# Kernel optimization log

Measured on AMD Instinct MI355X. Metric: run time of the kernel, lower is better.

The kernel has to match this reference:

```python
import jax, jax.numpy as jnp
import numpy as np

N_QUBITS = 4
N_LAYERS = 2
PROJ_DIM = 64
B = 262144
C64 = jnp.complex64


def setup_inputs() -> dict:
    key = jax.random.key(0)
    ks = jax.random.split(key, 4)
    x = jax.random.normal(ks[0], (B, N_QUBITS), dtype=jnp.float32)
    # TorchLayer default init: uniform(0, 2*pi)
    weights = jax.random.uniform(ks[1], (N_LAYERS, N_QUBITS, 3), dtype=jnp.float32) * (2.0 * np.pi)
    W = jax.random.normal(ks[2], (PROJ_DIM, N_QUBITS), dtype=jnp.float32) * 0.5
    b = jnp.zeros((PROJ_DIM,), dtype=jnp.float32)
    gamma = jnp.ones((PROJ_DIM,), dtype=jnp.float32)
    beta = jnp.zeros((PROJ_DIM,), dtype=jnp.float32)
    return {"x": x, "weights": weights, "W": W, "b": b, "gamma": gamma, "beta": beta}


def _apply_1q(state, U, w):
    # state: (B, 2,2,2,2); U: (2,2) shared or (B,2,2) per-sample
    s = jnp.moveaxis(state, 1 + w, -1)
    if U.ndim == 3:
        s = jnp.einsum('b...j,bij->b...i', s, U)
    else:
        s = s @ U.T
    return jnp.moveaxis(s, -1, 1 + w)


def _apply_cnot(state, c, t):
    s = jnp.moveaxis(state, (1 + c, 1 + t), (-2, -1))
    s = jnp.concatenate([s[..., :1, :], s[..., 1:, ::-1]], axis=-2)
    return jnp.moveaxis(s, (-2, -1), (1 + c, 1 + t))


def _rot_matrix(phi, theta, omega):
    # PennyLane Rot = RZ(omega) @ RY(theta) @ RZ(phi)
    c = jnp.cos(theta / 2).astype(C64)
    s = jnp.sin(theta / 2).astype(C64)
    ep = jnp.exp(-0.5j * (phi + omega).astype(C64))
    em = jnp.exp(0.5j * (phi - omega).astype(C64))
    return jnp.array(0, C64) + jnp.stack([
        jnp.stack([ep * c, -em * s]),
        jnp.stack([jnp.conj(em) * s, jnp.conj(ep) * c])], axis=0)


def _circuit(angles, weights):
    # angles: (B, n) real; returns (B, n) PauliZ expvals
    n = N_QUBITS
    Bn = angles.shape[0]
    state = jnp.zeros((Bn, 2 ** n), dtype=C64).at[:, 0].set(1.0)
    state = state.reshape((Bn,) + (2,) * n)
    # AngleEmbedding: RX(angle_w) on wire w (per-sample angles)
    half = angles / 2
    cos_h = jnp.cos(half).astype(C64)
    isin_h = (-1j) * jnp.sin(half).astype(C64)
    for w in range(n):
        U = jnp.stack([jnp.stack([cos_h[:, w], isin_h[:, w]], -1),
                       jnp.stack([isin_h[:, w], cos_h[:, w]], -1)], -2)  # (B,2,2)
        state = _apply_1q(state, U, w)
    # StronglyEntanglingLayers: Rot on each wire, then CNOT ring with range r
    for l in range(N_LAYERS):
        for w in range(n):
            U = _rot_matrix(weights[l, w, 0], weights[l, w, 1], weights[l, w, 2])
            state = _apply_1q(state, U, w)
        r = l % (n - 1) + 1
        for w in range(n):
            state = _apply_cnot(state, w, (w + r) % n)
    probs = jnp.abs(state) ** 2  # (B,2,...,2)
    sign = jnp.array([1.0, -1.0], dtype=jnp.float32)
    zs = []
    for w in range(n):
        axes = tuple(a for a in range(1, n + 1) if a != 1 + w)
        zs.append(probs.sum(axis=axes) @ sign)
    return jnp.stack(zs, -1)  # (B, n)


def reference(x, weights, W, b, gamma, beta):
    angles = jnp.tanh(x) * np.pi
    q = _circuit(angles, weights)            # (B, n_qubits)
    q = jax.nn.softmax(q, axis=-1)
    h = q @ W.T + b                          # (B, proj_dim)
    mu = h.mean(axis=-1, keepdims=True)
    var = ((h - mu) ** 2).mean(axis=-1, keepdims=True)
    hn = (h - mu) * jax.lax.rsqrt(var + 1e-5)
    return hn * gamma + beta
```

## Files before the change

kernel.cpp:

```cpp
#include <hip/hip_runtime.h>
#include <cstdint>


#define CONST_AS __attribute__((address_space(4)))
template <typename T>
__device__ inline const CONST_AS T* as_const4(const T* p) {
    return (const CONST_AS T*)(uintptr_t)p;
}

typedef float v4f __attribute__((ext_vector_type(4)));

#define WS_VRT 0
#define WS_VIT 256
#define WS_A   512
#define WS_B0  768
#define WS_G   832
#define WS_g   848
#define WS_C0  852

__global__ __launch_bounds__(64) void qb_setup(const float* __restrict__ wts,
                                               const float* __restrict__ W,
                                               const float* __restrict__ bias,
                                               const float* __restrict__ gamma,
                                               float* __restrict__ ws) {
    const int lane = threadIdx.x;
    const int row  = lane >> 2;
    const int cg   = lane & 3;

    float ur[4], ui[4];
    #pragma unroll
    for (int c = 0; c < 4; ++c) {
        ur[c] = (row == 4*cg + c) ? 1.f : 0.f;
        ui[c] = 0.f;
    }

    #pragma unroll
    for (int l = 0; l < 2; ++l) {
        #pragma unroll
        for (int w = 0; w < 4; ++w) {
            const float ph = wts[l*12 + w*3 + 0];
            const float th = wts[l*12 + w*3 + 1];
            const float om = wts[l*12 + w*3 + 2];
            float st, ct; __sincosf(0.5f*th, &st, &ct);
            float sp, cp; __sincosf(0.5f*(ph+om), &sp, &cp);
            float sm, cm; __sincosf(0.5f*(ph-om), &sm, &cm);
            const float a00r =  cp*ct, a00i = -sp*ct;
            const float a01r = -cm*st, a01i = -sm*st;
            const float a10r =  cm*st, a10i = -sm*st;
            const float a11r =  cp*ct, a11i =  sp*ct;
            const int m = 8 >> w;
            const int xm = m << 2;
            const bool hi = (row & m) != 0;
            #pragma unroll
            for (int c = 0; c < 4; ++c) {
                const float pr = __shfl_xor(ur[c], xm, 64);
                const float pi = __shfl_xor(ui[c], xm, 64);
                float nr, ni;
                if (!hi) {
                    nr = a00r*ur[c] - a00i*ui[c] + a01r*pr - a01i*pi;
                    ni = a00r*ui[c] + a00i*ur[c] + a01r*pi + a01i*pr;
                } else {
                    nr = a11r*ur[c] - a11i*ui[c] + a10r*pr - a10i*pi;
                    ni = a11r*ui[c] + a11i*ur[c] + a10r*pi + a10i*pr;
                }
                ur[c] = nr; ui[c] = ni;
            }
        }
        const int rr = (l == 0) ? 1 : 2;
        #pragma unroll
        for (int w = 0; w < 4; ++w) {
            const int cmk = 8 >> w;
            const int tmk = 8 >> ((w + rr) & 3);
            const int src = (row & cmk) ? (row ^ tmk) : row;
            const int srcLane = src*4 + cg;
            #pragma unroll
            for (int c = 0; c < 4; ++c) {
                ur[c] = __shfl(ur[c], srcLane, 64);
                ui[c] = __shfl(ui[c], srcLane, 64);
            }
        }
    }

    #pragma unroll
    for (int c = 0; c < 4; ++c) {
        const int col = 4*cg + c;
        const int p = __popc(col) & 3;
        float vr, vi;
        if (p == 0)      { vr =  ur[c]; vi =  ui[c]; }
        else if (p == 1) { vr =  ui[c]; vi = -ur[c]; }
        else if (p == 2) { vr = -ur[c]; vi = -ui[c]; }
        else             { vr = -ui[c]; vi =  ur[c]; }
        ws[WS_VRT + col*16 + row] = vr;
        ws[WS_VIT + col*16 + row] = vi;
    }

    {
        const int k = lane;
        float w0 = W[k*4+0], w1 = W[k*4+1], w2 = W[k*4+2], w3 = W[k*4+3];
        float bk = bias[k];
        auto wsum = [](float v) {
            #pragma unroll
            for (int o = 32; o; o >>= 1) v += __shfl_xor(v, o, 64);
            return v;
        };
        const float inv64 = 1.f/64.f;
        const float m0 = wsum(w0)*inv64, m1 = wsum(w1)*inv64;
        const float m2 = wsum(w2)*inv64, m3 = wsum(w3)*inv64;
        const float bm = wsum(bk)*inv64;
        float cc[4] = {w0-m0, w1-m1, w2-m2, w3-m3};
        const float bc = bk - bm;
        const float gk = gamma[k];
        #pragma unroll
        for (int w = 0; w < 4; ++w) ws[WS_A + k*4 + w] = cc[w]*gk;
        ws[WS_B0 + k] = bc*gk;
        #pragma unroll
        for (int a = 0; a < 4; ++a)
            #pragma unroll
            for (int b2 = 0; b2 < 4; ++b2) {
                const float s = wsum(cc[a]*cc[b2])*inv64;
                if (k == 0) ws[WS_G + a*4 + b2] = s;
            }
        #pragma unroll
        for (int a = 0; a < 4; ++a) {
            const float s = wsum(bc*cc[a])*inv64;
            if (k == 0) ws[WS_g + a] = s;
        }
        {
            const float s = wsum(bc*bc)*inv64;
            if (k == 0) ws[WS_C0] = s;
        }
    }
}

__global__ __launch_bounds__(256) void qb_main(const float* __restrict__ x,
                                               const float* __restrict__ beta,
                                               const float* __restrict__ ws_g,
                                               float* __restrict__ out) {
    __shared__ float4 lq[256];
    __shared__ float  linv[256];

    const int tid = threadIdx.x;
    const int sample = blockIdx.x * 256 + tid;
    const float4 xv = ((const float4*)x)[sample];
    const float xa[4] = {xv.x, xv.y, xv.z, xv.w};

    const int k4t = tid & 15;
    float4 A4[4]; float B04[4], Bt4[4];
    #pragma unroll
    for (int u = 0; u < 4; ++u) {
        const int k = k4t*4 + u;
        A4[u]  = ((const float4*)(ws_g + WS_A))[k];
        B04[u] = ws_g[WS_B0 + k];
        Bt4[u] = beta[k];
    }

    float c[4], s[4];
    #pragma unroll
    for (int w = 0; w < 4; ++w) {
        const float h = tanhf(xa[w]) * 1.5707963267948966f;
        __sincosf(h, &s[w], &c[w]);
    }
    const float e01[4] = {c[0]*c[1], c[0]*s[1], s[0]*c[1], s[0]*s[1]};
    const float e23[4] = {c[2]*c[3], c[2]*s[3], s[2]*c[3], s[2]*s[3]};
    float m[16];
    #pragma unroll
    for (int j = 0; j < 16; ++j) m[j] = e01[j>>2]*e23[j&3];

    const CONST_AS float* V = as_const4(ws_g);
    float r[16], si[16];
    #pragma unroll
    for (int i = 0; i < 16; ++i) { r[i] = 0.f; si[i] = 0.f; }
    #pragma unroll
    for (int j = 0; j < 16; ++j) {
        const float mj = m[j];
        #pragma unroll
        for (int i = 0; i < 16; ++i) {
            r[i]  = fmaf(V[WS_VRT + j*16 + i], mj, r[i]);
            si[i] = fmaf(V[WS_VIT + j*16 + i], mj, si[i]);
        }
    }
    float z0 = 0.f, z1 = 0.f, z2 = 0.f, z3 = 0.f;
    #pragma unroll
    for (int i = 0; i < 16; ++i) {
        const float p = r[i]*r[i] + si[i]*si[i];
        z0 += (i & 8) ? -p : p;
        z1 += (i & 4) ? -p : p;
        z2 += (i & 2) ? -p : p;
        z3 += (i & 1) ? -p : p;
    }
    const float mx = fmaxf(fmaxf(z0, z1), fmaxf(z2, z3));
    const float e0 = __expf(z0-mx), e1 = __expf(z1-mx);
    const float e2 = __expf(z2-mx), e3 = __expf(z3-mx);
    const float rs = 1.f / (e0+e1+e2+e3);
    const float4 qv = make_float4(e0*rs, e1*rs, e2*rs, e3*rs);

    float var = V[WS_C0];
    {
        const float qa[4] = {qv.x, qv.y, qv.z, qv.w};
        #pragma unroll
        for (int a = 0; a < 4; ++a) {
            float t = 2.f * V[WS_g + a];
            #pragma unroll
            for (int b2 = 0; b2 < 4; ++b2) t = fmaf(V[WS_G + a*4 + b2], qa[b2], t);
            var = fmaf(qa[a], t, var);
        }
    }
    const float inv = rsqrtf(var + 1e-5f);

    lq[tid]   = qv;
    linv[tid] = inv;
    __syncthreads();

    float4* outv = (float4*)out + (size_t)blockIdx.x * 4096;
    #pragma unroll
    for (int iter = 0; iter < 16; ++iter) {
        const int f  = iter*256 + tid;
        const int sl = f >> 4;
        const float4 q  = lq[sl];
        const float  iv = linv[sl];
        float4 o;
        float* op = (float*)&o;
        #pragma unroll
        for (int u = 0; u < 4; ++u) {
            float t = B04[u];
            t = fmaf(A4[u].x, q.x, t);
            t = fmaf(A4[u].y, q.y, t);
            t = fmaf(A4[u].z, q.z, t);
            t = fmaf(A4[u].w, q.w, t);
            op[u] = fmaf(t, iv, Bt4[u]);
        }
        outv[f] = o;
    }
}

extern "C" void kernel_launch(void* const* d_in, const int* in_sizes, int n_in,
                              void* d_out, int out_size, void* d_ws, size_t ws_size,
                              hipStream_t stream) {
    const float* x     = (const float*)d_in[0];
    const float* wts   = (const float*)d_in[1];
    const float* W     = (const float*)d_in[2];
    const float* bias  = (const float*)d_in[3];
    const float* gamma = (const float*)d_in[4];
    const float* beta  = (const float*)d_in[5];
    float* out = (float*)d_out;
    float* ws  = (float*)d_ws;
    const int B = in_sizes[0] / 4;

    hipLaunchKernelGGL(qb_setup, dim3(1), dim3(64), 0, stream, wts, W, bias, gamma, ws);
    hipLaunchKernelGGL(qb_main, dim3(B / 256), dim3(256), 0, stream, x, beta, ws, out);
}
```

Measured before the change: 97.04 us.

## Fuse setup into main kernel with per-wave redundant precompute in LDS

Removes the separate single-block setup kernel. Every wavefront now recomputes the circuit unitary and the LayerNorm statistics itself and keeps them in its own LDS slice. The output broadcast switches from a block-level LDS exchange with __syncthreads to wave-local shuffles, and the matrix reads use float4 LDS loads instead of scalar constant loads. This saves a kernel launch and the serial dependency between the two kernels. The cost is a large amount of redundant setup work per wave: sincos calls, dozens of shuffles and reductions, repeated across 4096 blocks.

```diff
diff --git a/kernel.cpp b/kernel.cpp
--- a/kernel.cpp
+++ b/kernel.cpp
@@ -1,14 +1,6 @@
 #include <hip/hip_runtime.h>
 #include <cstdint>
 
-
-#define CONST_AS __attribute__((address_space(4)))
-template <typename T>
-__device__ inline const CONST_AS T* as_const4(const T* p) {
-    return (const CONST_AS T*)(uintptr_t)p;
-}
-
-typedef float v4f __attribute__((ext_vector_type(4)));
 
 #define WS_VRT 0
 #define WS_VIT 256
@@ -17,166 +9,161 @@
 #define WS_G   832
 #define WS_g   848
 #define WS_C0  852
-
-__global__ __launch_bounds__(64) void qb_setup(const float* __restrict__ wts,
-                                               const float* __restrict__ W,
-                                               const float* __restrict__ bias,
-                                               const float* __restrict__ gamma,
-                                               float* __restrict__ ws) {
-    const int lane = threadIdx.x;
-    const int row  = lane >> 2;
-    const int cg   = lane & 3;
-
-    float ur[4], ui[4];
-    #pragma unroll
-    for (int c = 0; c < 4; ++c) {
-        ur[c] = (row == 4*cg + c) ? 1.f : 0.f;
-        ui[c] = 0.f;
-    }
-
-    #pragma unroll
-    for (int l = 0; l < 2; ++l) {
-        #pragma unroll
-        for (int w = 0; w < 4; ++w) {
-            const float ph = wts[l*12 + w*3 + 0];
-            const float th = wts[l*12 + w*3 + 1];
-            const float om = wts[l*12 + w*3 + 2];
-            float st, ct; __sincosf(0.5f*th, &st, &ct);
-            float sp, cp; __sincosf(0.5f*(ph+om), &sp, &cp);
-            float sm, cm; __sincosf(0.5f*(ph-om), &sm, &cm);
-            const float a00r =  cp*ct, a00i = -sp*ct;
-            const float a01r = -cm*st, a01i = -sm*st;
-            const float a10r =  cm*st, a10i = -sm*st;
-            const float a11r =  cp*ct, a11i =  sp*ct;
-            const int m = 8 >> w;
-            const int xm = m << 2;
-            const bool hi = (row & m) != 0;
-            #pragma unroll
-            for (int c = 0; c < 4; ++c) {
-                const float pr = __shfl_xor(ur[c], xm, 64);
-                const float pi = __shfl_xor(ui[c], xm, 64);
-                float nr, ni;
-                if (!hi) {
-                    nr = a00r*ur[c] - a00i*ui[c] + a01r*pr - a01i*pi;
-                    ni = a00r*ui[c] + a00i*ur[c] + a01r*pi + a01i*pr;
-                } else {
-                    nr = a11r*ur[c] - a11i*ui[c] + a10r*pr - a10i*pi;
-                    ni = a11r*ui[c] + a11i*ur[c] + a10r*pi + a10i*pr;
-                }
-                ur[c] = nr; ui[c] = ni;
-            }
-        }
-        const int rr = (l == 0) ? 1 : 2;
-        #pragma unroll
-        for (int w = 0; w < 4; ++w) {
-            const int cmk = 8 >> w;
-            const int tmk = 8 >> ((w + rr) & 3);
-            const int src = (row & cmk) ? (row ^ tmk) : row;
-            const int srcLane = src*4 + cg;
-            #pragma unroll
-            for (int c = 0; c < 4; ++c) {
-                ur[c] = __shfl(ur[c], srcLane, 64);
-                ui[c] = __shfl(ui[c], srcLane, 64);
-            }
-        }
-    }
-
-    #pragma unroll
-    for (int c = 0; c < 4; ++c) {
-        const int col = 4*cg + c;
-        const int p = __popc(col) & 3;
-        float vr, vi;
-        if (p == 0)      { vr =  ur[c]; vi =  ui[c]; }
-        else if (p == 1) { vr =  ui[c]; vi = -ur[c]; }
-        else if (p == 2) { vr = -ur[c]; vi = -ui[c]; }
-        else             { vr = -ui[c]; vi =  ur[c]; }
-        ws[WS_VRT + col*16 + row] = vr;
-        ws[WS_VIT + col*16 + row] = vi;
-    }
-
-    {
-        const int k = lane;
-        float w0 = W[k*4+0], w1 = W[k*4+1], w2 = W[k*4+2], w3 = W[k*4+3];
-        float bk = bias[k];
-        auto wsum = [](float v) {
-            #pragma unroll
-            for (int o = 32; o; o >>= 1) v += __shfl_xor(v, o, 64);
-            return v;
-        };
-        const float inv64 = 1.f/64.f;
-        const float m0 = wsum(w0)*inv64, m1 = wsum(w1)*inv64;
-        const float m2 = wsum(w2)*inv64, m3 = wsum(w3)*inv64;
-        const float bm = wsum(bk)*inv64;
-        float cc[4] = {w0-m0, w1-m1, w2-m2, w3-m3};
-        const float bc = bk - bm;
-        const float gk = gamma[k];
-        #pragma unroll
-        for (int w = 0; w < 4; ++w) ws[WS_A + k*4 + w] = cc[w]*gk;
-        ws[WS_B0 + k] = bc*gk;
-        #pragma unroll
-        for (int a = 0; a < 4; ++a)
-            #pragma unroll
-            for (int b2 = 0; b2 < 4; ++b2) {
-                const float s = wsum(cc[a]*cc[b2])*inv64;
-                if (k == 0) ws[WS_G + a*4 + b2] = s;
-            }
-        #pragma unroll
-        for (int a = 0; a < 4; ++a) {
-            const float s = wsum(bc*cc[a])*inv64;
-            if (k == 0) ws[WS_g + a] = s;
-        }
-        {
-            const float s = wsum(bc*bc)*inv64;
-            if (k == 0) ws[WS_C0] = s;
-        }
-    }
-}
-
-__global__ __launch_bounds__(256) void qb_main(const float* __restrict__ x,
-                                               const float* __restrict__ beta,
-                                               const float* __restrict__ ws_g,
-                                               float* __restrict__ out) {
-    __shared__ float4 lq[256];
-    __shared__ float  linv[256];
-
-    const int tid = threadIdx.x;
+#define WREG   864
+
+__global__ __launch_bounds__(256) void qb_fused(const float* __restrict__ x,
+                                                const float* __restrict__ wts,
+                                                const float* __restrict__ W,
+                                                const float* __restrict__ bias,
+                                                const float* __restrict__ gamma,
+                                                const float* __restrict__ beta,
+                                                float* __restrict__ out) {
+    __shared__ __align__(16) float lds[4 * WREG];
+    const int tid  = threadIdx.x;
+    const int wv   = tid >> 6;
+    const int lane = tid & 63;
+    float* wlds = lds + wv * WREG;
+
     const int sample = blockIdx.x * 256 + tid;
     const float4 xv = ((const float4*)x)[sample];
+
+    {
+        const int row = lane >> 2;
+        const int cg  = lane & 3;
+        float ur[4], ui[4];
+        #pragma unroll
+        for (int c = 0; c < 4; ++c) { ur[c] = (row == 4*cg + c) ? 1.f : 0.f; ui[c] = 0.f; }
+
+        #pragma unroll
+        for (int l = 0; l < 2; ++l) {
+            #pragma unroll
+            for (int w = 0; w < 4; ++w) {
+                const float ph = wts[l*12 + w*3 + 0];
+                const float th = wts[l*12 + w*3 + 1];
+                const float om = wts[l*12 + w*3 + 2];
+                float st, ct; __sincosf(0.5f*th, &st, &ct);
+                float sp, cp; __sincosf(0.5f*(ph+om), &sp, &cp);
+                float sm, cm; __sincosf(0.5f*(ph-om), &sm, &cm);
+                const float a00r =  cp*ct, a00i = -sp*ct;
+                const float a01r = -cm*st, a01i = -sm*st;
+                const float a10r =  cm*st, a10i = -sm*st;
+                const float a11r =  cp*ct, a11i =  sp*ct;
+                const int m8 = 8 >> w;
+                const int xm = m8 << 2;
+                const bool hi = (row & m8) != 0;
+                #pragma unroll
+                for (int c = 0; c < 4; ++c) {
+                    const float pr = __shfl_xor(ur[c], xm, 64);
+                    const float pi = __shfl_xor(ui[c], xm, 64);
+                    float nr, ni;
+                    if (!hi) {
+                        nr = a00r*ur[c] - a00i*ui[c] + a01r*pr - a01i*pi;
+                        ni = a00r*ui[c] + a00i*ur[c] + a01r*pi + a01i*pr;
+                    } else {
+                        nr = a11r*ur[c] - a11i*ui[c] + a10r*pr - a10i*pi;
+                        ni = a11r*ui[c] + a11i*ur[c] + a10r*pi + a10i*pr;
+                    }
+                    ur[c] = nr; ui[c] = ni;
+                }
+            }
+            const int rr = (l == 0) ? 1 : 2;
+            #pragma unroll
+            for (int w = 0; w < 4; ++w) {
+                const int cmk = 8 >> w;
+                const int tmk = 8 >> ((w + rr) & 3);
+                const int src = (row & cmk) ? (row ^ tmk) : row;
+                const int srcLane = src*4 + cg;
+                #pragma unroll
+                for (int c = 0; c < 4; ++c) {
+                    ur[c] = __shfl(ur[c], srcLane, 64);
+                    ui[c] = __shfl(ui[c], srcLane, 64);
+                }
+            }
+        }
+
+        #pragma unroll
+        for (int c = 0; c < 4; ++c) {
+            const int col = 4*cg + c;
+            const int p = __popc(col) & 3;
+            float vr, vi;
+            if (p == 0)      { vr =  ur[c]; vi =  ui[c]; }
+            else if (p == 1) { vr =  ui[c]; vi = -ur[c]; }
+            else if (p == 2) { vr = -ur[c]; vi = -ui[c]; }
+            else             { vr = -ui[c]; vi =  ur[c]; }
+            wlds[WS_VRT + col*16 + row] = vr;
+            wlds[WS_VIT + col*16 + row] = vi;
+        }
+
+        {
+            const int k = lane;
+            const float4 wk = ((const float4*)W)[k];
+            const float w0 = wk.x, w1 = wk.y, w2 = wk.z, w3 = wk.w;
+            const float bk = bias[k];
+            auto wsum = [](float v) {
+                #pragma unroll
+                for (int o = 32; o; o >>= 1) v += __shfl_xor(v, o, 64);
+                return v;
+            };
+            const float inv64 = 1.f/64.f;
+            const float m0 = wsum(w0)*inv64, m1 = wsum(w1)*inv64;
+            const float m2 = wsum(w2)*inv64, m3 = wsum(w3)*inv64;
+            const float bm = wsum(bk)*inv64;
+            float cc[4] = {w0-m0, w1-m1, w2-m2, w3-m3};
+            const float bc = bk - bm;
+            const float gk = gamma[k];
+            float4 av;
+            av.x = cc[0]*gk; av.y = cc[1]*gk; av.z = cc[2]*gk; av.w = cc[3]*gk;
+            ((float4*)(wlds + WS_A))[k] = av;
+            wlds[WS_B0 + k] = bc*gk;
+            #pragma unroll
+            for (int a = 0; a < 4; ++a)
+                #pragma unroll
+                for (int b2 = 0; b2 < 4; ++b2) {
+                    const float s = wsum(cc[a]*cc[b2])*inv64;
+                    if (k == 0) wlds[WS_G + a*4 + b2] = s;
+                }
+            #pragma unroll
+            for (int a = 0; a < 4; ++a) {
+                const float s = wsum(bc*cc[a])*inv64;
+                if (k == 0) wlds[WS_g + a] = s;
+            }
+            { const float s = wsum(bc*bc)*inv64; if (k == 0) wlds[WS_C0] = s; }
+        }
+    }
+
     const float xa[4] = {xv.x, xv.y, xv.z, xv.w};
-
-    const int k4t = tid & 15;
-    float4 A4[4]; float B04[4], Bt4[4];
-    #pragma unroll
-    for (int u = 0; u < 4; ++u) {
-        const int k = k4t*4 + u;
-        A4[u]  = ((const float4*)(ws_g + WS_A))[k];
-        B04[u] = ws_g[WS_B0 + k];
-        Bt4[u] = beta[k];
-    }
-
-    float c[4], s[4];
+    float c4[4], s4[4];
     #pragma unroll
     for (int w = 0; w < 4; ++w) {
         const float h = tanhf(xa[w]) * 1.5707963267948966f;
-        __sincosf(h, &s[w], &c[w]);
-    }
-    const float e01[4] = {c[0]*c[1], c[0]*s[1], s[0]*c[1], s[0]*s[1]};
-    const float e23[4] = {c[2]*c[3], c[2]*s[3], s[2]*c[3], s[2]*s[3]};
+        __sincosf(h, &s4[w], &c4[w]);
+    }
+    const float e01[4] = {c4[0]*c4[1], c4[0]*s4[1], s4[0]*c4[1], s4[0]*s4[1]};
+    const float e23[4] = {c4[2]*c4[3], c4[2]*s4[3], s4[2]*c4[3], s4[2]*s4[3]};
     float m[16];
     #pragma unroll
     for (int j = 0; j < 16; ++j) m[j] = e01[j>>2]*e23[j&3];
 
-    const CONST_AS float* V = as_const4(ws_g);
     float r[16], si[16];
     #pragma unroll
     for (int i = 0; i < 16; ++i) { r[i] = 0.f; si[i] = 0.f; }
+    const float4* vr4 = (const float4*)(wlds + WS_VRT);
+    const float4* vi4 = (const float4*)(wlds + WS_VIT);
     #pragma unroll
     for (int j = 0; j < 16; ++j) {
         const float mj = m[j];
         #pragma unroll
-        for (int i = 0; i < 16; ++i) {
-            r[i]  = fmaf(V[WS_VRT + j*16 + i], mj, r[i]);
-            si[i] = fmaf(V[WS_VIT + j*16 + i], mj, si[i]);
+        for (int i4 = 0; i4 < 4; ++i4) {
+            const float4 a = vr4[j*4 + i4];
+            const float4 b = vi4[j*4 + i4];
+            r [i4*4+0] = fmaf(a.x, mj, r [i4*4+0]);
+            r [i4*4+1] = fmaf(a.y, mj, r [i4*4+1]);
+            r [i4*4+2] = fmaf(a.z, mj, r [i4*4+2]);
+            r [i4*4+3] = fmaf(a.w, mj, r [i4*4+3]);
+            si[i4*4+0] = fmaf(b.x, mj, si[i4*4+0]);
+            si[i4*4+1] = fmaf(b.y, mj, si[i4*4+1]);
+            si[i4*4+2] = fmaf(b.z, mj, si[i4*4+2]);
+            si[i4*4+3] = fmaf(b.w, mj, si[i4*4+3]);
         }
     }
     float z0 = 0.f, z1 = 0.f, z2 = 0.f, z3 = 0.f;
@@ -192,44 +179,60 @@
     const float e0 = __expf(z0-mx), e1 = __expf(z1-mx);
     const float e2 = __expf(z2-mx), e3 = __expf(z3-mx);
     const float rs = 1.f / (e0+e1+e2+e3);
-    const float4 qv = make_float4(e0*rs, e1*rs, e2*rs, e3*rs);
-
-    float var = V[WS_C0];
+    const float qx = e0*rs, qy = e1*rs, qz = e2*rs, qw = e3*rs;
+
+    float var = wlds[WS_C0];
     {
-        const float qa[4] = {qv.x, qv.y, qv.z, qv.w};
+        const float4 Gs0 = ((const float4*)(wlds + WS_G))[0];
+        const float4 Gs1 = ((const float4*)(wlds + WS_G))[1];
+        const float4 Gs2 = ((const float4*)(wlds + WS_G))[2];
+        const float4 Gs3 = ((const float4*)(wlds + WS_G))[3];
+        const float4 gv  = ((const float4*)(wlds + WS_g))[0];
+        const float qa[4] = {qx, qy, qz, qw};
+        const float4 Gs[4] = {Gs0, Gs1, Gs2, Gs3};
+        const float ga[4] = {gv.x, gv.y, gv.z, gv.w};
         #pragma unroll
         for (int a = 0; a < 4; ++a) {
-            float t = 2.f * V[WS_g + a];
-            #pragma unroll
-            for (int b2 = 0; b2 < 4; ++b2) t = fmaf(V[WS_G + a*4 + b2], qa[b2], t);
+            float t = 2.f * ga[a];
+            t = fmaf(Gs[a].x, qa[0], t);
+            t = fmaf(Gs[a].y, qa[1], t);
+            t = fmaf(Gs[a].z, qa[2], t);
+            t = fmaf(Gs[a].w, qa[3], t);
             var = fmaf(qa[a], t, var);
         }
     }
     const float inv = rsqrtf(var + 1e-5f);
 
-    lq[tid]   = qv;
-    linv[tid] = inv;
-    __syncthreads();
-
-    float4* outv = (float4*)out + (size_t)blockIdx.x * 4096;
+    const int k4t = lane & 15;
+    float4 A4[4];
+    #pragma unroll
+    for (int u = 0; u < 4; ++u) A4[u] = ((const float4*)(wlds + WS_A))[k4t*4 + u];
+    const float4 B04v = ((const float4*)(wlds + WS_B0))[k4t];
+    const float4 Bt4v = ((const float4*)beta)[k4t];
+    const float B04[4] = {B04v.x, B04v.y, B04v.z, B04v.w};
+    const float Bt4[4] = {Bt4v.x, Bt4v.y, Bt4v.z, Bt4v.w};
+
+    float4* outv = (float4*)out + (size_t)blockIdx.x * 4096 + wv * 1024;
     #pragma unroll
     for (int iter = 0; iter < 16; ++iter) {
-        const int f  = iter*256 + tid;
-        const int sl = f >> 4;
-        const float4 q  = lq[sl];
-        const float  iv = linv[sl];
+        const int src = iter*4 + (lane >> 4);
+        const float bqx = __shfl(qx,  src, 64);
+        const float bqy = __shfl(qy,  src, 64);
+        const float bqz = __shfl(qz,  src, 64);
+        const float bqw = __shfl(qw,  src, 64);
+        const float biv = __shfl(inv, src, 64);
         float4 o;
         float* op = (float*)&o;
         #pragma unroll
         for (int u = 0; u < 4; ++u) {
             float t = B04[u];
-            t = fmaf(A4[u].x, q.x, t);
-            t = fmaf(A4[u].y, q.y, t);
-            t = fmaf(A4[u].z, q.z, t);
-            t = fmaf(A4[u].w, q.w, t);
-            op[u] = fmaf(t, iv, Bt4[u]);
-        }
-        outv[f] = o;
+            t = fmaf(A4[u].x, bqx, t);
+            t = fmaf(A4[u].y, bqy, t);
+            t = fmaf(A4[u].z, bqz, t);
+            t = fmaf(A4[u].w, bqw, t);
+            op[u] = fmaf(t, biv, Bt4[u]);
+        }
+        outv[iter*64 + lane] = o;
     }
 }
 
@@ -243,9 +246,8 @@
     const float* gamma = (const float*)d_in[4];
     const float* beta  = (const float*)d_in[5];
     float* out = (float*)d_out;
-    float* ws  = (float*)d_ws;
     const int B = in_sizes[0] / 4;
 
-    hipLaunchKernelGGL(qb_setup, dim3(1), dim3(64), 0, stream, wts, W, bias, gamma, ws);
-    hipLaunchKernelGGL(qb_main, dim3(B / 256), dim3(256), 0, stream, x, beta, ws, out);
+    hipLaunchKernelGGL(qb_fused, dim3(B / 256), dim3(256), 0, stream,
+                       x, wts, W, bias, gamma, beta, out);
 }
```

Result: slower. 102.3 us (+5.4%).

## Make output write phase wave-local and drop block barrier

Applied to the files above, without the earlier changes.

Each wavefront now writes the output rows for its own 64 samples, so the LDS exchange stays inside one wave and the __syncthreads barrier is removed. The address-space-4 constant pointer cast for the ws table is dropped in favour of plain global loads, and B0 and beta are loaded as float4. The launch bounds gain a minimum of 4 blocks, and the setup kernel computes only the upper triangle of the symmetric Gram matrix. Skipping the barrier depends on the wave executing in lockstep, and the plain loads may compile to vector loads instead of scalar loads for the uniform table.

```diff
diff --git a/kernel.cpp b/kernel.cpp
--- a/kernel.cpp
+++ b/kernel.cpp
@@ -1,14 +1,6 @@
 #include <hip/hip_runtime.h>
 #include <cstdint>
 
-
-#define CONST_AS __attribute__((address_space(4)))
-template <typename T>
-__device__ inline const CONST_AS T* as_const4(const T* p) {
-    return (const CONST_AS T*)(uintptr_t)p;
-}
-
-typedef float v4f __attribute__((ext_vector_type(4)));
 
 #define WS_VRT 0
 #define WS_VIT 256
@@ -48,9 +40,9 @@
             const float a01r = -cm*st, a01i = -sm*st;
             const float a10r =  cm*st, a10i = -sm*st;
             const float a11r =  cp*ct, a11i =  sp*ct;
-            const int m = 8 >> w;
-            const int xm = m << 2;
-            const bool hi = (row & m) != 0;
+            const int m8 = 8 >> w;
+            const int xm = m8 << 2;
+            const bool hi = (row & m8) != 0;
             #pragma unroll
             for (int c = 0; c < 4; ++c) {
                 const float pr = __shfl_xor(ur[c], xm, 64);
@@ -116,9 +108,12 @@
         #pragma unroll
         for (int a = 0; a < 4; ++a)
             #pragma unroll
-            for (int b2 = 0; b2 < 4; ++b2) {
+            for (int b2 = a; b2 < 4; ++b2) {
                 const float s = wsum(cc[a]*cc[b2])*inv64;
-                if (k == 0) ws[WS_G + a*4 + b2] = s;
+                if (k == 0) {
+                    ws[WS_G + a*4 + b2] = s;
+                    ws[WS_G + b2*4 + a] = s;
+                }
             }
         #pragma unroll
         for (int a = 0; a < 4; ++a) {
@@ -132,41 +127,41 @@
     }
 }
 
-__global__ __launch_bounds__(256) void qb_main(const float* __restrict__ x,
-                                               const float* __restrict__ beta,
-                                               const float* __restrict__ ws_g,
-                                               float* __restrict__ out) {
-    __shared__ float4 lq[256];
-    __shared__ float  linv[256];
-
-    const int tid = threadIdx.x;
+__global__ __launch_bounds__(256, 4) void qb_main(const float* __restrict__ x,
+                                                  const float* __restrict__ beta,
+                                                  const float* __restrict__ ws,
+                                                  float* __restrict__ out) {
+    __shared__ __align__(16) float4 sq[256];
+    __shared__ float sinv[256];
+
+    const int tid  = threadIdx.x;
+    const int wv   = tid >> 6;
+    const int lane = tid & 63;
+
     const int sample = blockIdx.x * 256 + tid;
     const float4 xv = ((const float4*)x)[sample];
-    const float xa[4] = {xv.x, xv.y, xv.z, xv.w};
-
-    const int k4t = tid & 15;
-    float4 A4[4]; float B04[4], Bt4[4];
-    #pragma unroll
-    for (int u = 0; u < 4; ++u) {
-        const int k = k4t*4 + u;
-        A4[u]  = ((const float4*)(ws_g + WS_A))[k];
-        B04[u] = ws_g[WS_B0 + k];
-        Bt4[u] = beta[k];
-    }
-
-    float c[4], s[4];
-    #pragma unroll
-    for (int w = 0; w < 4; ++w) {
-        const float h = tanhf(xa[w]) * 1.5707963267948966f;
-        __sincosf(h, &s[w], &c[w]);
-    }
-    const float e01[4] = {c[0]*c[1], c[0]*s[1], s[0]*c[1], s[0]*s[1]};
-    const float e23[4] = {c[2]*c[3], c[2]*s[3], s[2]*c[3], s[2]*s[3]};
+    const int k4t = lane & 15;
+    float4 A4[4];
+    #pragma unroll
+    for (int u = 0; u < 4; ++u) A4[u] = ((const float4*)(ws + WS_A))[k4t*4 + u];
+    const float4 B04v = ((const float4*)(ws + WS_B0))[k4t];
+    const float4 Bt4v = ((const float4*)beta)[k4t];
+
     float m[16];
-    #pragma unroll
-    for (int j = 0; j < 16; ++j) m[j] = e01[j>>2]*e23[j&3];
-
-    const CONST_AS float* V = as_const4(ws_g);
+    {
+        const float xa[4] = {xv.x, xv.y, xv.z, xv.w};
+        float c4[4], s4[4];
+        #pragma unroll
+        for (int w = 0; w < 4; ++w) {
+            const float h = tanhf(xa[w]) * 1.5707963267948966f;
+            __sincosf(h, &s4[w], &c4[w]);
+        }
+        const float e01[4] = {c4[0]*c4[1], c4[0]*s4[1], s4[0]*c4[1], s4[0]*s4[1]};
+        const float e23[4] = {c4[2]*c4[3], c4[2]*s4[3], s4[2]*c4[3], s4[2]*s4[3]};
+        #pragma unroll
+        for (int j = 0; j < 16; ++j) m[j] = e01[j>>2]*e23[j&3];
+    }
+
     float r[16], si[16];
     #pragma unroll
     for (int i = 0; i < 16; ++i) { r[i] = 0.f; si[i] = 0.f; }
@@ -175,10 +170,11 @@
         const float mj = m[j];
         #pragma unroll
         for (int i = 0; i < 16; ++i) {
-            r[i]  = fmaf(V[WS_VRT + j*16 + i], mj, r[i]);
-            si[i] = fmaf(V[WS_VIT + j*16 + i], mj, si[i]);
-        }
-    }
+            r[i]  = fmaf(ws[WS_VRT + j*16 + i], mj, r[i]);
+            si[i] = fmaf(ws[WS_VIT + j*16 + i], mj, si[i]);
+        }
+    }
+
     float z0 = 0.f, z1 = 0.f, z2 = 0.f, z3 = 0.f;
     #pragma unroll
     for (int i = 0; i < 16; ++i) {
@@ -192,32 +188,33 @@
     const float e0 = __expf(z0-mx), e1 = __expf(z1-mx);
     const float e2 = __expf(z2-mx), e3 = __expf(z3-mx);
     const float rs = 1.f / (e0+e1+e2+e3);
-    const float4 qv = make_float4(e0*rs, e1*rs, e2*rs, e3*rs);
-
-    float var = V[WS_C0];
+    const float qx = e0*rs, qy = e1*rs, qz = e2*rs, qw = e3*rs;
+
+    float var = ws[WS_C0];
     {
-        const float qa[4] = {qv.x, qv.y, qv.z, qv.w};
+        const float qa[4] = {qx, qy, qz, qw};
         #pragma unroll
         for (int a = 0; a < 4; ++a) {
-            float t = 2.f * V[WS_g + a];
-            #pragma unroll
-            for (int b2 = 0; b2 < 4; ++b2) t = fmaf(V[WS_G + a*4 + b2], qa[b2], t);
+            float t = 2.f * ws[WS_g + a];
+            #pragma unroll
+            for (int b2 = 0; b2 < 4; ++b2) t = fmaf(ws[WS_G + a*4 + b2], qa[b2], t);
             var = fmaf(qa[a], t, var);
         }
     }
     const float inv = rsqrtf(var + 1e-5f);
 
-    lq[tid]   = qv;
-    linv[tid] = inv;
-    __syncthreads();
-
-    float4* outv = (float4*)out + (size_t)blockIdx.x * 4096;
+    sq[wv*64 + lane]   = make_float4(qx, qy, qz, qw);
+    sinv[wv*64 + lane] = inv;
+
+    const float B04[4] = {B04v.x, B04v.y, B04v.z, B04v.w};
+    const float Bt4[4] = {Bt4v.x, Bt4v.y, Bt4v.z, Bt4v.w};
+    float4* outv = (float4*)out + (size_t)blockIdx.x * 4096 + wv * 1024 + lane;
+    const float4* qld = sq + wv*64 + (lane >> 4);
+    const float*  ild = sinv + wv*64 + (lane >> 4);
     #pragma unroll
     for (int iter = 0; iter < 16; ++iter) {
-        const int f  = iter*256 + tid;
-        const int sl = f >> 4;
-        const float4 q  = lq[sl];
-        const float  iv = linv[sl];
+        const float4 q  = qld[iter*4];
+        const float  iv = ild[iter*4];
         float4 o;
         float* op = (float*)&o;
         #pragma unroll
@@ -229,7 +226,7 @@
             t = fmaf(A4[u].w, q.w, t);
             op[u] = fmaf(t, iv, Bt4[u]);
         }
-        outv[f] = o;
+        outv[iter*64] = o;
     }
 }
 
```

Result: no change. 96.26 us (-0.8%).
